# Kernel tuning notes

Measured on AMD Instinct MI355X. Metric: run time of the kernel, lower is better.

Reference implementation:

```python
import jax, jax.numpy as jnp
import numpy as np

N, E, QL, HID = 1024, 8192, 8, 1024
NH, NKV, HD = 16, 8, 64          # heads, kv heads, head_dim; groups = NH // NKV = 2
INTER = 4096
THETA = 10000.0
EPS = 1e-6


def rmsnorm(x, w):
    v = x.astype(jnp.float32)
    v = v * jax.lax.rsqrt(jnp.mean(v * v, axis=-1, keepdims=True) + EPS)
    return w * v.astype(x.dtype)


def rotate_half(x):
    h = x.shape[-1] // 2
    return jnp.concatenate([-x[..., h:], x[..., :h]], axis=-1)


def rope_tables(seq_len):
    inv_freq = 1.0 / (THETA ** (jnp.arange(0, HD, 2, dtype=jnp.float32) / HD))
    freqs = jnp.arange(seq_len, dtype=jnp.float32)[:, None] * inv_freq[None, :]
    emb = jnp.concatenate([freqs, freqs], axis=-1)  # [seq_len, HD]
    return jnp.cos(emb), jnp.sin(emb)


def setup_inputs() -> dict:
    key = jax.random.key(0)
    ks = jax.random.split(key, 14)
    w = lambda k, sh: (jax.random.normal(k, sh, jnp.float32) * 0.02)
    return {
        "hidden_states": jax.random.normal(ks[0], (N, QL, HID), jnp.float32),
        "edge_index": jax.random.randint(ks[1], (2, E), 0, N, dtype=jnp.int32),
        "edge_hidden_states": jax.random.normal(ks[2], (E, QL, HID), jnp.float32),
        "Wq": w(ks[3], (NH * HD, HID)),
        "Wk": w(ks[4], (NKV * HD, HID)),
        "Wv": w(ks[5], (NKV * HD, HID)),
        "Wo": w(ks[6], (HID, HID)),
        "Wgate": w(ks[7], (INTER, HID)),
        "Wup": w(ks[8], (INTER, HID)),
        "Wdown": w(ks[9], (HID, INTER)),
        "ln1_w": jnp.ones((HID,), jnp.float32),
        "ln2_w": jnp.ones((HID,), jnp.float32),
    }


def gofa_layer(hidden_states, edge_index, edge_hidden_states, Wq, Wk, Wv, Wo,
               Wgate, Wup, Wdown, ln1_w, ln2_w):
    src, dst = edge_index[0], edge_index[1]  # message flows src -> dst
    residual = hidden_states
    x = rmsnorm(hidden_states, ln1_w)  # [N, QL, HID]

    q = x @ Wq.T                     # [N, QL, NH*HD]
    k = x @ Wk.T                     # [N, QL, NKV*HD]
    v = x @ Wv.T
    ek = edge_hidden_states @ Wk.T   # [E, QL, NKV*HD]
    ev = edge_hidden_states @ Wv.T

    # per-edge gather
    q_i = q[dst]                     # [E, QL, NH*HD]
    k_j, v_j = k[src], v[src]        # [E, QL, NKV*HD]

    # interleave node/edge tokens: [E, 2*QL, NKV*HD]
    keys = jnp.stack([k_j, ek], axis=2).reshape(E, 2 * QL, NKV * HD)
    vals = jnp.stack([v_j, ev], axis=2).reshape(E, 2 * QL, NKV * HD)

    qh = q_i.reshape(E, QL, NH, HD).transpose(0, 2, 1, 3)        # [E, NH, QL, HD]
    kh = keys.reshape(E, 2 * QL, NKV, HD).transpose(0, 2, 1, 3)  # [E, NKV, 2QL, HD]
    vh = vals.reshape(E, 2 * QL, NKV, HD).transpose(0, 2, 1, 3)

    cos_k, sin_k = rope_tables(2 * QL)
    cos_q, sin_q = cos_k[:QL], sin_k[:QL]
    qh = qh * cos_q[None, None] + rotate_half(qh) * sin_q[None, None]
    kh = kh * cos_k[None, None] + rotate_half(kh) * sin_k[None, None]

    groups = NH // NKV
    kh = jnp.repeat(kh, groups, axis=1)  # [E, NH, 2QL, HD]
    vh = jnp.repeat(vh, groups, axis=1)

    logits = jnp.einsum('ehqd,ehkd->ehqk', qh, kh) / np.sqrt(HD)  # [E, NH, QL, 2QL]

    # segment softmax over (edges into same dst node) x (2QL key positions)
    seg = jnp.repeat(dst, 2 * QL)                                  # [E*2QL]
    a = logits.transpose(0, 3, 1, 2).reshape(E * 2 * QL, NH, QL)   # [E*2QL, NH, QL]
    m = jax.ops.segment_max(a, seg, num_segments=N)                # [N, NH, QL]
    ex = jnp.exp(a - m[seg])
    s = jax.ops.segment_sum(ex, seg, num_segments=N)
    alpha = ex / (s[seg] + 1e-16)
    alpha = alpha.reshape(E, 2 * QL, NH, QL).transpose(0, 2, 3, 1)  # [E, NH, QL, 2QL]

    out_e = jnp.einsum('ehqk,ehkd->ehqd', alpha, vh)               # [E, NH, QL, HD]
    out_e = out_e.transpose(0, 2, 1, 3).reshape(E, QL, HID)

    agg = jax.ops.segment_sum(out_e, dst, num_segments=N)          # [N, QL, HID]
    attn_out = agg @ Wo.T

    h = residual + attn_out
    h2 = rmsnorm(h, ln2_w)
    mlp = (jax.nn.silu(h2 @ Wgate.T) * (h2 @ Wup.T)) @ Wdown.T
    return h + mlp


def reference(hidden_states, edge_index, edge_hidden_states, Wq, Wk, Wv, Wo,
              Wgate, Wup, Wdown, ln1_w, ln2_w):
    return gofa_layer(hidden_states, edge_index, edge_hidden_states, Wq, Wk, Wv,
                      Wo, Wgate, Wup, Wdown, ln1_w, ln2_w)
```

## Files before the change

### kernel.cpp

```cpp
#include <hip/hip_runtime.h>
#include <cstddef>
#include <cstdint>

constexpr int kN    = 1024;
constexpr int kE    = 8192;
constexpr int kQL   = 8;
constexpr int kHID  = 1024;

typedef __bf16 bf16x8 __attribute__((ext_vector_type(8)));
typedef float  f32x4  __attribute__((ext_vector_type(4)));
typedef unsigned short ushort8 __attribute__((ext_vector_type(8)));

__device__ __forceinline__ unsigned short f2bf(float f) {
  unsigned u = __float_as_uint(f);
  unsigned r = (u + 0x7FFFu + ((u >> 16) & 1u)) >> 16;
  return (unsigned short)r;
}
__device__ __forceinline__ float bf2f(unsigned short u) {
  return __uint_as_float((unsigned)u << 16);
}
__device__ __forceinline__ unsigned pkbf(float a, float b) {
  return (unsigned)f2bf(a) | ((unsigned)f2bf(b) << 16);
}
__device__ __forceinline__ void gload_lds16(const void* g, void* l) {
  __builtin_amdgcn_global_load_lds(
      (const __attribute__((address_space(1))) void*)g,
      (__attribute__((address_space(3))) void*)l, 16, 0, 0);
}

__global__ void rope_tables_kernel(float* __restrict__ ct, float* __restrict__ st) {
  int i = threadIdx.x;
  int p = i >> 5, j = i & 31;
  float inv = expf(-((float)(2 * j) / 64.0f) * logf(10000.0f));
  float ang = (float)p * inv;
  ct[i] = cosf(ang);
  st[i] = sinf(ang);
}

__global__ __launch_bounds__(256) void cvt_kernel(
    const float* __restrict__ in, unsigned short* __restrict__ out, int n8) {
  int i = blockIdx.x * 256 + threadIdx.x;
  if (i >= n8) return;
  const float4* p = (const float4*)(in + (size_t)i * 8);
  float4 a = p[0], b = p[1];
  uint4 o;
  o.x = f2bf(a.x) | ((unsigned)f2bf(a.y) << 16);
  o.y = f2bf(a.z) | ((unsigned)f2bf(a.w) << 16);
  o.z = f2bf(b.x) | ((unsigned)f2bf(b.y) << 16);
  o.w = f2bf(b.z) | ((unsigned)f2bf(b.w) << 16);
  *(uint4*)(out + (size_t)i * 8) = o;
}

__global__ __launch_bounds__(256) void cvt_gu_kernel(
    const float* __restrict__ Wg, const float* __restrict__ Wu,
    unsigned short* __restrict__ out) {
  int i = blockIdx.x * 256 + threadIdx.x;
  int n = i >> 7, ck = (i & 127) * 8;
  int isUp = (n >> 4) & 1;
  int srow = (n >> 6) * 32 + ((n >> 5) & 1) * 16 + (n & 15);
  const float* src = (isUp ? Wu : Wg) + (size_t)srow * 1024 + ck;
  const float4* p = (const float4*)src;
  float4 a = p[0], b = p[1];
  uint4 o;
  o.x = f2bf(a.x) | ((unsigned)f2bf(a.y) << 16);
  o.y = f2bf(a.z) | ((unsigned)f2bf(a.w) << 16);
  o.z = f2bf(b.x) | ((unsigned)f2bf(b.y) << 16);
  o.w = f2bf(b.z) | ((unsigned)f2bf(b.w) << 16);
  *(uint4*)(out + (size_t)n * 1024 + ck) = o;
}

__global__ __launch_bounds__(256) void rmsnorm_bf16_kernel(
    const float* __restrict__ in, const float* __restrict__ w,
    unsigned short* __restrict__ out) {
  __shared__ float red[4];
  int row = blockIdx.x, tid = threadIdx.x;
  const float* p = in + (size_t)row * kHID + tid * 4;
  float4 v = *(const float4*)p;
  float ss = v.x*v.x + v.y*v.y + v.z*v.z + v.w*v.w;
  #pragma unroll
  for (int off = 32; off > 0; off >>= 1) ss += __shfl_down(ss, off);
  int lane = tid & 63, wv = tid >> 6;
  if (lane == 0) red[wv] = ss;
  __syncthreads();
  float tot = red[0] + red[1] + red[2] + red[3];
  float rn = rsqrtf(tot * (1.0f / (float)kHID) + 1e-6f);
  float4 w4 = *(const float4*)(w + tid * 4);
  uint2 o;
  o.x = f2bf(v.x*rn*w4.x) | ((unsigned)f2bf(v.y*rn*w4.y) << 16);
  o.y = f2bf(v.z*rn*w4.z) | ((unsigned)f2bf(v.w*rn*w4.w) << 16);
  *(uint2*)(out + (size_t)row * kHID + tid * 4) = o;
}

template<int OUTMODE>
__global__ __launch_bounds__(512, 2) void gemm8p(
    const unsigned short* __restrict__ A, const unsigned short* __restrict__ B,
    const float* __restrict__ resid, void* __restrict__ Cout,
    const float* __restrict__ ct, const float* __restrict__ st,
    int M, int N, int K) {
  __shared__ unsigned short As[2][2][128][64];
  __shared__ unsigned short Bs[2][2][128][64];
  const int tid = threadIdx.x;
  const int lane = tid & 63, wid = tid >> 6;
  const int gx = gridDim.x;
  int id = blockIdx.y * gx + blockIdx.x;
  {
    const int nwg = gx * gridDim.y;
    const int cpx = nwg >> 3;
    id = (id & 7) * cpx + (id >> 3);
  }
  const int m0 = (id / gx) * 256, n0 = (id % gx) * 256;
  const int wr = wid >> 2, wc = wid & 3;
  const int l15 = lane & 15, lg = lane >> 4;
  const int swz = l15 & 7;
  const int NT = K >> 6;

  const int scol = ((lane & 7) ^ (lane >> 3)) * 8;
  const unsigned short* Asrc = A + (size_t)(m0 + wid * 16 + (lane >> 3)) * K + scol;
  const unsigned short* Bsrc = B + (size_t)(n0 + wid * 16 + (lane >> 3)) * K + scol;
  const size_t rK8 = (size_t)8 * K, rK128 = (size_t)128 * K;
  const int brow0 = (wc & 1) * 64;

#define STAGEA(t_, h_, b_) do {                                              \
    gload_lds16(Asrc + (size_t)(h_) * rK128 + (size_t)(t_) * 64,             \
                (unsigned short*)&As[b_][h_][0][0] + (wid * 2 + 0) * 512);   \
    gload_lds16(Asrc + (size_t)(h_) * rK128 + rK8 + (size_t)(t_) * 64,       \
                (unsigned short*)&As[b_][h_][0][0] + (wid * 2 + 1) * 512);   \
  } while (0)
#define STAGEB(t_, h_, b_) do {                                              \
    gload_lds16(Bsrc + (size_t)(h_) * rK128 + (size_t)(t_) * 64,             \
                (unsigned short*)&Bs[b_][h_][0][0] + (wid * 2 + 0) * 512);   \
    gload_lds16(Bsrc + (size_t)(h_) * rK128 + rK8 + (size_t)(t_) * 64,       \
                (unsigned short*)&Bs[b_][h_][0][0] + (wid * 2 + 1) * 512);   \
  } while (0)

  bf16x8 afr[2][4], bfr[2][4];
#define LOADA(b_, qm_) do {                                                  \
    _Pragma("unroll") for (int kk = 0; kk < 2; ++kk)                         \
    _Pragma("unroll") for (int mi = 0; mi < 4; ++mi)                         \
      afr[kk][mi] = *(const bf16x8*)&As[b_][wr][((qm_) * 4 + mi) * 16 + l15] \
                                       [((kk * 4 + lg) ^ swz) * 8];          \
  } while (0)
#define LOADB(b_, qn_) do {                                                  \
    _Pragma("unroll") for (int kk = 0; kk < 2; ++kk)                         \
    _Pragma("unroll") for (int nj = 0; nj < 2; ++nj)                         \
      bfr[kk][(qn_) * 2 + nj] =                                              \
        *(const bf16x8*)&Bs[b_][wc >> 1][brow0 + ((qn_) * 2 + nj) * 16 + l15]\
                           [((kk * 4 + lg) ^ swz) * 8];                      \
  } while (0)

  f32x4 acc[8][4] = {};
#define MFMAQ(qm_, qn_) do {                                                 \
    __builtin_amdgcn_s_setprio(1);                                           \
    _Pragma("unroll") for (int mi = 0; mi < 4; ++mi)                         \
    _Pragma("unroll") for (int nj = 0; nj < 2; ++nj) {                       \
      acc[(qm_) * 4 + mi][(qn_) * 2 + nj] =                                  \
        __builtin_amdgcn_mfma_f32_16x16x32_bf16(afr[0][mi],                  \
          bfr[0][(qn_) * 2 + nj], acc[(qm_) * 4 + mi][(qn_) * 2 + nj], 0,0,0);\
      acc[(qm_) * 4 + mi][(qn_) * 2 + nj] =                                  \
        __builtin_amdgcn_mfma_f32_16x16x32_bf16(afr[1][mi],                  \
          bfr[1][(qn_) * 2 + nj], acc[(qm_) * 4 + mi][(qn_) * 2 + nj], 0,0,0);\
    }                                                                        \
    __builtin_amdgcn_s_setprio(0);                                           \
  } while (0)

#define BAR_PRE() do {                                                       \
    __builtin_amdgcn_sched_barrier(0);                                       \
    __builtin_amdgcn_s_barrier();                                            \
    asm volatile("s_waitcnt lgkmcnt(0)" ::: "memory");                       \
    __builtin_amdgcn_sched_barrier(0);                                       \
  } while (0)
#define BAR_POST() do {                                                      \
    __builtin_amdgcn_sched_barrier(0);                                       \
    __builtin_amdgcn_s_barrier();                                            \
    __builtin_amdgcn_sched_barrier(0);                                       \
  } while (0)

  STAGEA(0, 0, 0); STAGEA(0, 1, 0); STAGEB(0, 0, 0); STAGEB(0, 1, 0);
  STAGEB(1, 0, 1); STAGEB(1, 1, 1);
  asm volatile("s_waitcnt vmcnt(4)" ::: "memory");
  __builtin_amdgcn_sched_barrier(0);
  __builtin_amdgcn_s_barrier();
  __builtin_amdgcn_sched_barrier(0);

  for (int t0 = 0; t0 < NT; t0 += 2) {
    const bool more = (t0 + 2 < NT);
    LOADA(0, 0); LOADB(0, 0);
    STAGEA(t0 + 1, 0, 1);
    BAR_PRE(); MFMAQ(0, 0); BAR_POST();
    LOADB(0, 1);
    STAGEA(t0 + 1, 1, 1);
    BAR_PRE(); MFMAQ(0, 1); BAR_POST();
    LOADA(0, 1);
    if (more) STAGEB(t0 + 2, 0, 0);
    BAR_PRE(); MFMAQ(1, 0); BAR_POST();
    if (more) {
      asm volatile("s_waitcnt vmcnt(2)" ::: "memory");
      STAGEB(t0 + 2, 1, 0);
    } else {
      asm volatile("s_waitcnt vmcnt(0)" ::: "memory");
    }
    BAR_PRE(); MFMAQ(1, 1); BAR_POST();
    LOADA(1, 0); LOADB(1, 0);
    if (more) STAGEA(t0 + 2, 0, 0);
    BAR_PRE(); MFMAQ(0, 0); BAR_POST();
    LOADB(1, 1);
    if (more) STAGEA(t0 + 2, 1, 0);
    BAR_PRE(); MFMAQ(0, 1); BAR_POST();
    LOADA(1, 1);
    if (more) STAGEB(t0 + 3, 0, 1);
    BAR_PRE(); MFMAQ(1, 0); BAR_POST();
    if (more) {
      asm volatile("s_waitcnt vmcnt(2)" ::: "memory");
      STAGEB(t0 + 3, 1, 1);
    }
    BAR_PRE(); MFMAQ(1, 1); BAR_POST();
  }
#undef STAGEA
#undef STAGEB
#undef LOADA
#undef LOADB
#undef MFMAQ
#undef BAR_PRE
#undef BAR_POST

  const int r0 = lg * 4;
  const int bc = n0 + wc * 64;
  #pragma unroll
  for (int mi = 0; mi < 8; ++mi) {
    #pragma unroll
    for (int r = 0; r < 4; ++r) {
      const size_t grow = (size_t)(m0 + wr * 128 + mi * 16 + r0 + r);
      if (OUTMODE == 0) {
        #pragma unroll
        for (int nj = 0; nj < 4; ++nj) {
          const size_t gi = grow * N + (bc + nj * 16 + l15);
          float v = acc[mi][nj][r];
          if (resid) v += resid[gi];
          ((float*)Cout)[gi] = v;
        }
      } else if (OUTMODE == 2) {
        #pragma unroll
        for (int p = 0; p < 2; ++p) {
          float gv = acc[mi][2 * p][r], uv = acc[mi][2 * p + 1][r];
          float res = gv / (1.f + __expf(-gv)) * uv;
          ((unsigned short*)Cout)[grow * (size_t)(N >> 1) + (bc >> 1) + p * 16 + l15] = f2bf(res);
        }
      } else {
        bool doR = false; int pos = 0;
        if (OUTMODE == 3) { doR = bc < 512; pos = 2 * ((int)grow & 7) + 1; }
        if (OUTMODE == 4) {
          if (bc < 1024)      { doR = true; pos = (int)grow & 7; }
          else if (bc < 1536) { doR = true; pos = 2 * ((int)grow & 7); }
        }
        unsigned short* o16 = (unsigned short*)Cout;
        if (doR) {
          #pragma unroll
          for (int nj = 0; nj < 2; ++nj) {
            float a = acc[mi][nj][r], b = acc[mi][nj + 2][r];
            float c = ct[pos * 32 + nj * 16 + l15];
            float s = st[pos * 32 + nj * 16 + l15];
            o16[grow * N + bc + nj * 16 + l15]       = f2bf(a * c - b * s);
            o16[grow * N + bc + (nj + 2) * 16 + l15] = f2bf(b * c + a * s);
          }
        } else {
          #pragma unroll
          for (int nj = 0; nj < 4; ++nj)
            o16[grow * N + bc + nj * 16 + l15] = f2bf(acc[mi][nj][r]);
        }
      }
    }
  }
}

__global__ void csr_count_kernel(const int* __restrict__ dst, int* __restrict__ cnt) {
  int e = blockIdx.x * 256 + threadIdx.x;
  if (e < kE) atomicAdd(&cnt[dst[e]], 1);
}
__global__ __launch_bounds__(1024) void csr_scan_kernel(
    const int* __restrict__ cnt, int* __restrict__ start) {
  __shared__ int tmp[1024];
  int t = threadIdx.x;
  tmp[t] = cnt[t];
  __syncthreads();
  for (int off = 1; off < 1024; off <<= 1) {
    int add = (t >= off) ? tmp[t - off] : 0;
    __syncthreads();
    tmp[t] += add;
    __syncthreads();
  }
  start[t + 1] = tmp[t];
  if (t == 0) start[0] = 0;
}
__global__ void csr_scatter_kernel(const int* __restrict__ dst, const int* __restrict__ start,
                                   int* __restrict__ cursor, int* __restrict__ elist) {
  int e = blockIdx.x * 256 + threadIdx.x;
  if (e < kE) {
    int d = dst[e];
    int pos = atomicAdd(&cursor[d], 1);
    elist[start[d] + pos] = e;
  }
}

__global__ __launch_bounds__(256) void attn_mfma_kernel(
    const unsigned short* __restrict__ qkv,
    const unsigned short* __restrict__ ekv,
    const int* __restrict__ srcIdx, const int* __restrict__ elist,
    const int* __restrict__ start,
    unsigned short* __restrict__ aggb) {
  const int n = blockIdx.x >> 1;
  const int g = (blockIdx.x & 1) * 4 + (threadIdx.x >> 6);
  const int lane = threadIdx.x & 63;
  const int l15 = lane & 15, lg = lane >> 4;

  const int h = g * 2 + (l15 >> 3), q = l15 & 7;
  const unsigned short* qrow = qkv + ((size_t)n * 8 + q) * 2048 + h * 64 + lg * 8;
  const bf16x8 qf0 = *(const bf16x8*)qrow;
  const bf16x8 qf1 = *(const bf16x8*)(qrow + 32);

  float m = -3.4e38f, sh = 0.f;
  f32x4 oacc[4];
  #pragma unroll
  for (int t = 0; t < 4; ++t) oacc[t] = (f32x4){0.f, 0.f, 0.f, 0.f};

  const int kparity = l15 & 1;
  const int t_ = l15 >> 1;
  const int lgh = lg & 1;
  const int eS = lg >> 1;

  const int s0 = start[n], s1 = start[n + 1];
  for (int jj = s0; jj < s1; jj += 2) {
    const int e0 = elist[jj];
    const bool has1 = (jj + 1 < s1);
    const int e1 = has1 ? elist[jj + 1] : e0;
    const int sn0 = srcIdx[e0], sn1 = srcIdx[e1];

    const unsigned short* kr0 = kparity
        ? ekv + ((size_t)e0 * 8 + t_) * 1024 + g * 64 + lg * 8
        : qkv + ((size_t)sn0 * 8 + t_) * 2048 + 1024 + g * 64 + lg * 8;
    const unsigned short* kr1 = kparity
        ? ekv + ((size_t)e1 * 8 + t_) * 1024 + g * 64 + lg * 8
        : qkv + ((size_t)sn1 * 8 + t_) * 2048 + 1024 + g * 64 + lg * 8;
    bf16x8 ka0 = *(const bf16x8*)kr0, ka1 = *(const bf16x8*)(kr0 + 32);
    bf16x8 kc0 = *(const bf16x8*)kr1, kc1 = *(const bf16x8*)(kr1 + 32);

    const int evsel = eS ? e1 : e0;
    const int snsel = eS ? sn1 : sn0;
    const unsigned short* vn = qkv + ((size_t)snsel * 8 + lgh * 4) * 2048 + 1536 + g * 64;
    const unsigned short* ve = ekv + ((size_t)evsel * 8 + lgh * 4) * 1024 + 512 + g * 64;

    f32x4 z = (f32x4){0.f, 0.f, 0.f, 0.f};
    f32x4 sa = __builtin_amdgcn_mfma_f32_16x16x32_bf16(ka0, qf0, z, 0, 0, 0);
    sa       = __builtin_amdgcn_mfma_f32_16x16x32_bf16(ka1, qf1, sa, 0, 0, 0);
    f32x4 sb = __builtin_amdgcn_mfma_f32_16x16x32_bf16(kc0, qf0, z, 0, 0, 0);
    sb       = __builtin_amdgcn_mfma_f32_16x16x32_bf16(kc1, qf1, sb, 0, 0, 0);

    float l0[4], l1[4];
    float lmax = -3.4e38f;
    #pragma unroll
    for (int r = 0; r < 4; ++r) {
      l0[r] = sa[r] * 0.125f;
      l1[r] = has1 ? sb[r] * 0.125f : -3.4e38f;
      lmax = fmaxf(lmax, fmaxf(l0[r], l1[r]));
    }
    lmax = fmaxf(lmax, __shfl_xor(lmax, 16));
    lmax = fmaxf(lmax, __shfl_xor(lmax, 32));
    const float mnew = fmaxf(m, lmax);
    const float scale = __expf(m - mnew);
    float p0[4], p1[4], ps = 0.f;
    #pragma unroll
    for (int r = 0; r < 4; ++r) {
      p0[r] = __expf(l0[r] - mnew);
      p1[r] = __expf(l1[r] - mnew);
      ps += p0[r] + p1[r];
    }
    ps += __shfl_xor(ps, 16);
    ps += __shfl_xor(ps, 32);
    sh = sh * scale + ps;
    m = mnew;

    #pragma unroll
    for (int r = 0; r < 4; ++r) {
      float sr = __shfl(scale, lg * 4 + r);
      #pragma unroll
      for (int t = 0; t < 4; ++t) oacc[t][r] *= sr;
    }

    unsigned w00 = pkbf(p0[0], p0[1]), w01 = pkbf(p0[2], p0[3]);
    unsigned w10 = pkbf(p1[0], p1[1]), w11 = pkbf(p1[2], p1[3]);
    const int L1 = l15 + 32 * lgh, L2 = L1 + 16;
    unsigned a0 = __shfl(w00, L1), a1 = __shfl(w01, L1);
    unsigned a2 = __shfl(w00, L2), a3 = __shfl(w01, L2);
    unsigned b0 = __shfl(w10, L1), b1 = __shfl(w11, L1);
    unsigned b2 = __shfl(w10, L2), b3 = __shfl(w11, L2);
    uint4 wv;
    wv.x = eS ? b0 : a0; wv.y = eS ? b1 : a1;
    wv.z = eS ? b2 : a2; wv.w = eS ? b3 : a3;
    const bf16x8 pf = __builtin_bit_cast(bf16x8, wv);

    #pragma unroll
    for (int t = 0; t < 4; ++t) {
      const int col = t * 16 + l15;
      ushort8 vr;
      #pragma unroll
      for (int j = 0; j < 8; ++j)
        vr[j] = (j & 1) ? ve[(j >> 1) * 1024 + col] : vn[(j >> 1) * 2048 + col];
      const bf16x8 vf = __builtin_bit_cast(bf16x8, vr);
      oacc[t] = __builtin_amdgcn_mfma_f32_16x16x32_bf16(pf, vf, oacc[t], 0, 0, 0);
    }
  }

  #pragma unroll
  for (int r = 0; r < 4; ++r) {
    const float sr = __shfl(sh, lg * 4 + r);
    const float inv = 1.f / (sr + 1e-16f);
    const int hq = lg * 4 + r;
    const int hh = g * 2 + (hq >> 3), qq = hq & 7;
    unsigned short* op = aggb + ((size_t)n * 8 + qq) * 1024 + hh * 64 + l15;
    #pragma unroll
    for (int t = 0; t < 4; ++t) op[t * 16] = f2bf(oacc[t][r] * inv);
  }
}

extern "C" void kernel_launch(void* const* d_in, const int* in_sizes, int n_in,
                              void* d_out, int out_size, void* d_ws, size_t ws_size,
                              hipStream_t stream) {
  const float* hidden = (const float*)d_in[0];
  const int*   eidx   = (const int*)d_in[1];
  const float* ehid   = (const float*)d_in[2];
  const float* Wq     = (const float*)d_in[3];
  const float* Wk     = (const float*)d_in[4];
  const float* Wv     = (const float*)d_in[5];
  const float* Wo     = (const float*)d_in[6];
  const float* Wgate  = (const float*)d_in[7];
  const float* Wup    = (const float*)d_in[8];
  const float* Wdown  = (const float*)d_in[9];
  const float* ln1    = (const float*)d_in[10];
  const float* ln2    = (const float*)d_in[11];
  const int* srcIdx = eidx;
  const int* dstIdx = eidx + kE;

  char* wsb = (char*)d_ws;
  size_t off = 0;
  auto alloc = [&](size_t bytes) { char* p = wsb + off; off += (bytes + 255) & ~(size_t)255; return p; };
  unsigned short* eh16   = (unsigned short*)alloc(134217728);
  unsigned short* ekv16  = (unsigned short*)alloc(134217728);
  unsigned short* qkv16  = (unsigned short*)alloc(33554432);
  unsigned short* x16    = (unsigned short*)alloc(16777216);
  unsigned short* agg16  = (unsigned short*)alloc(16777216);
  float*          hbuf   = (float*)alloc(33554432);
  unsigned short* wqkv16 = (unsigned short*)alloc(4194304);
  unsigned short* wo16   = (unsigned short*)alloc(2097152);
  unsigned short* wgu16  = (unsigned short*)alloc(16777216);
  unsigned short* wd16   = (unsigned short*)alloc(8388608);
  int* cnt    = (int*)alloc(4096);
  int* cursor = (int*)alloc(4096);
  int* startb = (int*)alloc(4352);
  int* elist  = (int*)alloc(32768);
  float* ct   = (float*)alloc(2048);
  float* st   = (float*)alloc(2048);
  unsigned short* gm16 = ekv16;
  unsigned short* h216 = x16;
  float* outp = (float*)d_out;

  hipMemsetAsync(cnt, 0, 8192, stream);
  rope_tables_kernel<<<1, 512, 0, stream>>>(ct, st);

  cvt_kernel<<<32768, 256, 0, stream>>>(ehid,  eh16, 8388608);
  cvt_kernel<<<512,   256, 0, stream>>>(Wq,    wqkv16,                 131072);
  cvt_kernel<<<256,   256, 0, stream>>>(Wk,    wqkv16 + 1024 * 1024,   65536);
  cvt_kernel<<<256,   256, 0, stream>>>(Wv,    wqkv16 + 1536 * 1024,   65536);
  cvt_kernel<<<512,   256, 0, stream>>>(Wo,    wo16,                  131072);
  cvt_gu_kernel<<<4096, 256, 0, stream>>>(Wgate, Wup, wgu16);
  cvt_kernel<<<2048,  256, 0, stream>>>(Wdown, wd16,                  524288);

  csr_count_kernel<<<32, 256, 0, stream>>>(dstIdx, cnt);
  csr_scan_kernel<<<1, 1024, 0, stream>>>(cnt, startb);
  csr_scatter_kernel<<<32, 256, 0, stream>>>(dstIdx, startb, cursor, elist);

  rmsnorm_bf16_kernel<<<kN * kQL, 256, 0, stream>>>(hidden, ln1, x16);

  gemm8p<4><<<dim3(8, 32),  512, 0, stream>>>(x16,  wqkv16, nullptr, qkv16, ct, st, 8192, 2048, 1024);
  gemm8p<3><<<dim3(4, 256), 512, 0, stream>>>(eh16, wqkv16 + 1024 * 1024, nullptr, ekv16, ct, st, 65536, 1024, 1024);

  attn_mfma_kernel<<<2048, 256, 0, stream>>>(qkv16, ekv16, srcIdx, elist, startb, agg16);

  gemm8p<0><<<dim3(4, 32), 512, 0, stream>>>(agg16, wo16, hidden, hbuf, ct, st, 8192, 1024, 1024);

  rmsnorm_bf16_kernel<<<kN * kQL, 256, 0, stream>>>(hbuf, ln2, h216);
  gemm8p<2><<<dim3(32, 32), 512, 0, stream>>>(h216, wgu16, nullptr, gm16, ct, st, 8192, 8192, 1024);
  gemm8p<0><<<dim3(4, 32), 512, 0, stream>>>(gm16, wd16, hbuf, outp, ct, st, 8192, 1024, 4096);
}
```

Measured before the change: 787.8 us.

## Add smaller-tile triple-buffered GEMM for N=1024 projections to fill all CUs

Introduces a new GEMM kernel with 128x128 (or 256x128) tiles, a three-stage LDS pipeline and higher occupancy launch bounds. It is used for the output projection and the down projection, raising the grid from 128 to 512 workgroups. The aim is to stop leaving compute units idle on these N=1024 GEMMs. The trade-off is less data reuse per tile and more redundant global loads of the operands.

```diff
diff --git a/kernel.cpp b/kernel.cpp
--- a/kernel.cpp
+++ b/kernel.cpp
@@ -230,6 +230,132 @@
     #pragma unroll
     for (int r = 0; r < 4; ++r) {
       const size_t grow = (size_t)(m0 + wr * 128 + mi * 16 + r0 + r);
+      if (OUTMODE == 0) {
+        #pragma unroll
+        for (int nj = 0; nj < 4; ++nj) {
+          const size_t gi = grow * N + (bc + nj * 16 + l15);
+          float v = acc[mi][nj][r];
+          if (resid) v += resid[gi];
+          ((float*)Cout)[gi] = v;
+        }
+      } else if (OUTMODE == 2) {
+        #pragma unroll
+        for (int p = 0; p < 2; ++p) {
+          float gv = acc[mi][2 * p][r], uv = acc[mi][2 * p + 1][r];
+          float res = gv / (1.f + __expf(-gv)) * uv;
+          ((unsigned short*)Cout)[grow * (size_t)(N >> 1) + (bc >> 1) + p * 16 + l15] = f2bf(res);
+        }
+      } else {
+        bool doR = false; int pos = 0;
+        if (OUTMODE == 3) { doR = bc < 512; pos = 2 * ((int)grow & 7) + 1; }
+        if (OUTMODE == 4) {
+          if (bc < 1024)      { doR = true; pos = (int)grow & 7; }
+          else if (bc < 1536) { doR = true; pos = 2 * ((int)grow & 7); }
+        }
+        unsigned short* o16 = (unsigned short*)Cout;
+        if (doR) {
+          #pragma unroll
+          for (int nj = 0; nj < 2; ++nj) {
+            float a = acc[mi][nj][r], b = acc[mi][nj + 2][r];
+            float c = ct[pos * 32 + nj * 16 + l15];
+            float s = st[pos * 32 + nj * 16 + l15];
+            o16[grow * N + bc + nj * 16 + l15]       = f2bf(a * c - b * s);
+            o16[grow * N + bc + (nj + 2) * 16 + l15] = f2bf(b * c + a * s);
+          }
+        } else {
+          #pragma unroll
+          for (int nj = 0; nj < 4; ++nj)
+            o16[grow * N + bc + nj * 16 + l15] = f2bf(acc[mi][nj][r]);
+        }
+      }
+    }
+  }
+}
+
+template<int OUTMODE, int TM>
+__global__ __launch_bounds__(512, 4) void gemmk(
+    const unsigned short* __restrict__ A, const unsigned short* __restrict__ B,
+    const float* __restrict__ resid, void* __restrict__ Cout,
+    const float* __restrict__ ct, const float* __restrict__ st,
+    int M, int N, int K) {
+  constexpr int ABUFE = TM * 32;
+  constexpr int BBUFE = 128 * 32;
+  constexpr int WRS   = TM / 4;
+  constexpr int MI    = WRS / 16;
+  constexpr int LPS   = (TM == 256) ? 3 : 2;
+  __shared__ unsigned short As[3 * ABUFE];
+  __shared__ unsigned short Bs[3 * BBUFE];
+  const int tid = threadIdx.x;
+  const int lane = tid & 63, wid = tid >> 6;
+  const int gx = gridDim.x;
+  int id = blockIdx.y * gx + blockIdx.x;
+  {
+    const int nwg = gx * gridDim.y;
+    const int cpx = nwg >> 3;
+    id = (id & 7) * cpx + (id >> 3);
+  }
+  const int m0 = (id / gx) * TM, n0 = (id % gx) * 128;
+  const int wr = wid >> 1, wc = wid & 1;
+  const int l15 = lane & 15, lg = lane >> 4;
+  const int NT = K >> 5;
+
+  const int sr4 = lane >> 2, sc = lane & 3;
+  const int arow0 = (TM == 256) ? (wid * 32 + sr4) : (wid * 16 + sr4);
+  const int brow0 = wid * 16 + sr4;
+  const unsigned short* Asrc = A + (size_t)(m0 + arow0) * K + (sc ^ ((arow0 >> 1) & 3)) * 8;
+  const unsigned short* Bsrc = B + (size_t)(n0 + brow0) * K + (sc ^ ((brow0 >> 1) & 3)) * 8;
+  const size_t rK16 = (size_t)16 * K;
+
+#define STAGE(t_, b_) do {                                                   \
+    const size_t _k0 = (size_t)(t_) * 32;                                    \
+    if (TM == 256) {                                                         \
+      gload_lds16(Asrc + _k0,        As + (b_) * ABUFE + wid * 1024);        \
+      gload_lds16(Asrc + rK16 + _k0, As + (b_) * ABUFE + wid * 1024 + 512);  \
+    } else {                                                                 \
+      gload_lds16(Asrc + _k0,        As + (b_) * ABUFE + wid * 512);         \
+    }                                                                        \
+    gload_lds16(Bsrc + _k0,          Bs + (b_) * BBUFE + wid * 512);         \
+  } while (0)
+
+  f32x4 acc[MI][4] = {};
+  STAGE(0, 0); STAGE(1, 1);
+
+  const int rck = (lg ^ ((l15 >> 1) & 3)) * 8;
+  int cur = 0, nx2 = 2;
+  for (int t = 0; t < NT; ++t) {
+    __builtin_amdgcn_sched_barrier(0);
+    if (t + 1 < NT) asm volatile("s_waitcnt vmcnt(%0)" :: "i"(LPS) : "memory");
+    else            asm volatile("s_waitcnt vmcnt(0)" ::: "memory");
+    __builtin_amdgcn_s_barrier();
+    __builtin_amdgcn_sched_barrier(0);
+    if (t + 2 < NT) STAGE(t + 2, nx2);
+
+    const unsigned short* Ab = As + cur * ABUFE + (wr * WRS + l15) * 32 + rck;
+    const unsigned short* Bb = Bs + cur * BBUFE + (wc * 64 + l15) * 32 + rck;
+    bf16x8 af[MI], bf[4];
+    #pragma unroll
+    for (int mi = 0; mi < MI; ++mi) af[mi] = *(const bf16x8*)(Ab + mi * 512);
+    #pragma unroll
+    for (int nj = 0; nj < 4; ++nj) bf[nj] = *(const bf16x8*)(Bb + nj * 512);
+    __builtin_amdgcn_s_setprio(1);
+    #pragma unroll
+    for (int mi = 0; mi < MI; ++mi)
+      #pragma unroll
+      for (int nj = 0; nj < 4; ++nj)
+        acc[mi][nj] = __builtin_amdgcn_mfma_f32_16x16x32_bf16(af[mi], bf[nj], acc[mi][nj], 0, 0, 0);
+    __builtin_amdgcn_s_setprio(0);
+    cur = (cur == 2) ? 0 : cur + 1;
+    nx2 = (nx2 == 2) ? 0 : nx2 + 1;
+  }
+#undef STAGE
+
+  const int r0 = lg * 4;
+  const int bc = n0 + wc * 64;
+  #pragma unroll
+  for (int mi = 0; mi < MI; ++mi) {
+    #pragma unroll
+    for (int r = 0; r < 4; ++r) {
+      const size_t grow = (size_t)(m0 + wr * WRS + mi * 16 + r0 + r);
       if (OUTMODE == 0) {
         #pragma unroll
         for (int nj = 0; nj < 4; ++nj) {
@@ -484,9 +610,9 @@
 
   attn_mfma_kernel<<<2048, 256, 0, stream>>>(qkv16, ekv16, srcIdx, elist, startb, agg16);
 
-  gemm8p<0><<<dim3(4, 32), 512, 0, stream>>>(agg16, wo16, hidden, hbuf, ct, st, 8192, 1024, 1024);
+  gemmk<0, 128><<<dim3(8, 64), 512, 0, stream>>>(agg16, wo16, hidden, hbuf, ct, st, 8192, 1024, 1024);
 
   rmsnorm_bf16_kernel<<<kN * kQL, 256, 0, stream>>>(hbuf, ln2, h216);
   gemm8p<2><<<dim3(32, 32), 512, 0, stream>>>(h216, wgu16, nullptr, gm16, ct, st, 8192, 8192, 1024);
-  gemm8p<0><<<dim3(4, 32), 512, 0, stream>>>(gm16, wd16, hbuf, outp, ct, st, 8192, 1024, 4096);
-}
+  gemmk<0, 128><<<dim3(8, 64), 512, 0, stream>>>(gm16, wd16, hbuf, outp, ct, st, 8192, 1024, 4096);
+}
```

New measurement: 682.5 us. 13.4% less time.
